# Kernel optimization log

Measured on AMD Instinct MI355X. Metric: run time of the kernel, lower is better.

The kernel has to match this reference:

```python
import jax, jax.numpy as jnp
import numpy as np

C = 256
R = 16  # reduction
CR = C // R
LN_EPS = 1e-5


def setup_inputs() -> dict:
    key = jax.random.key(0)
    ks = jax.random.split(key, 8)
    B, H, W = 16, 128, 128
    x = jax.random.normal(ks[0], (B, C, H, W), dtype=jnp.float32)
    # conv_mask: Conv2d(C, 1, 1x1)
    w_mask = jax.random.normal(ks[1], (C,), dtype=jnp.float32) * (1.0 / np.sqrt(C))
    b_mask = jnp.zeros((), dtype=jnp.float32)
    # channel_add[0]: Conv2d(C, C//R, 1x1)
    w1 = jax.random.normal(ks[2], (CR, C), dtype=jnp.float32) * (1.0 / np.sqrt(C))
    b1 = jnp.zeros((CR,), dtype=jnp.float32)
    # channel_add[1]: LayerNorm([C//R, 1, 1])
    ln_g = jnp.ones((CR,), dtype=jnp.float32)
    ln_b = jnp.zeros((CR,), dtype=jnp.float32)
    # channel_add[3]: Conv2d(C//R, C, 1x1)
    w2 = jax.random.normal(ks[3], (C, CR), dtype=jnp.float32) * (1.0 / np.sqrt(CR))
    b2 = jnp.zeros((C,), dtype=jnp.float32)
    return {"x": x, "w_mask": w_mask, "b_mask": b_mask,
            "w1": w1, "b1": b1, "ln_g": ln_g, "ln_b": ln_b,
            "w2": w2, "b2": b2}


def reference(x, w_mask, b_mask, w1, b1, ln_g, ln_b, w2, b2):
    B, Cc, H, W = x.shape
    # 1x1 conv to 1 channel -> attention logits over H*W
    logits = jnp.einsum('bchw,c->bhw', x, w_mask) + b_mask          # [B,H,W]
    attn = jax.nn.softmax(logits.reshape(B, H * W), axis=-1)        # [B,HW]
    # attention-pooled global context: [B,C]
    context = jnp.einsum('bchw,bs->bc', x, attn.reshape(B, H, W).reshape(B, H * W)[:, :].reshape(B, H * W)) if False else jnp.einsum('bcs,bs->bc', x.reshape(B, Cc, H * W), attn)
    # channel_add MLP: conv1x1 -> LayerNorm over [C//R] -> ReLU -> conv1x1
    t = jnp.einsum('oc,bc->bo', w1, context) + b1                   # [B,C//R]
    mu = jnp.mean(t, axis=-1, keepdims=True)
    var = jnp.mean((t - mu) ** 2, axis=-1, keepdims=True)
    t = (t - mu) / jnp.sqrt(var + LN_EPS) * ln_g + ln_b
    t = jax.nn.relu(t)
    add = jnp.einsum('oc,bc->bo', w2, t) + b2                       # [B,C]
    return x + add[:, :, None, None]
```

## Files before the change

### kernel.cpp

```cpp
#include <hip/hip_runtime.h>
#include <math.h>

#define CC   256
#define CR   16
#define SB   16384
#define NB   16
#define ST   64
#define NT   (SB/ST)
#define LN_EPS 1e-5f

typedef float vfloat4 __attribute__((ext_vector_type(4)));

__global__ __launch_bounds__(256) void k_ctx_partial(const float* __restrict__ x,
                                                     const float* __restrict__ w_mask,
                                                     float* __restrict__ pc,
                                                     float* __restrict__ pm,
                                                     float* __restrict__ ps) {
    __shared__ float plog[ST * 5];
    __shared__ float pl[ST];
    __shared__ float wm[CC];
    __shared__ float red2[CC * 17];

    const int t   = threadIdx.x;
    const int bid = blockIdx.x;
    const int b   = bid / NT;
    const int s0  = (bid % NT) * ST;

    wm[t] = w_mask[t];
    __syncthreads();

    const int g  = t >> 4;
    const int i  = t & 15;
    const int s4 = i << 2;

    const float* xb = x + (size_t)b * CC * SB + s0 + s4;
    float4 v[16];
    float4 acc = make_float4(0.f, 0.f, 0.f, 0.f);
#pragma unroll
    for (int k = 0; k < 16; ++k) {
        const int c = g + (k << 4);
        v[k] = *reinterpret_cast<const float4*>(xb + (size_t)c * SB);
        const float w = wm[c];
        acc.x += v[k].x * w; acc.y += v[k].y * w;
        acc.z += v[k].z * w; acc.w += v[k].w * w;
    }
    acc.x += __shfl_xor(acc.x, 16); acc.y += __shfl_xor(acc.y, 16);
    acc.z += __shfl_xor(acc.z, 16); acc.w += __shfl_xor(acc.w, 16);
    acc.x += __shfl_xor(acc.x, 32); acc.y += __shfl_xor(acc.y, 32);
    acc.z += __shfl_xor(acc.z, 32); acc.w += __shfl_xor(acc.w, 32);
    const int wv = t >> 6;
    if ((t & 63) < 16) {
        plog[(s4 + 0) * 5 + wv] = acc.x;
        plog[(s4 + 1) * 5 + wv] = acc.y;
        plog[(s4 + 2) * 5 + wv] = acc.z;
        plog[(s4 + 3) * 5 + wv] = acc.w;
    }
    __syncthreads();

    if (t < ST) {
        const float logit = plog[t * 5 + 0] + plog[t * 5 + 1]
                          + plog[t * 5 + 2] + plog[t * 5 + 3];
        float m = logit;
#pragma unroll
        for (int off = 32; off > 0; off >>= 1)
            m = fmaxf(m, __shfl_xor(m, off));
        const float p = __expf(logit - m);
        pl[t] = p;
        float sum = p;
#pragma unroll
        for (int off = 32; off > 0; off >>= 1)
            sum += __shfl_xor(sum, off);
        if (t == 0) { pm[bid] = m; ps[bid] = sum; }
    }
    __syncthreads();

    const float p0 = pl[s4 + 0], p1 = pl[s4 + 1];
    const float p2 = pl[s4 + 2], p3 = pl[s4 + 3];
#pragma unroll
    for (int k = 0; k < 16; ++k) {
        const int c = g + (k << 4);
        red2[c * 17 + i] = v[k].x * p0 + v[k].y * p1 + v[k].z * p2 + v[k].w * p3;
    }
    __syncthreads();

    float s = 0.f;
#pragma unroll
    for (int j = 0; j < 16; ++j) s += red2[t * 17 + j];
    pc[(size_t)bid * CC + t] = s;
}

__global__ __launch_bounds__(256) void k_combine_mlp(const float* __restrict__ pc,
                                                     const float* __restrict__ pm,
                                                     const float* __restrict__ ps,
                                                     const float* __restrict__ w1,
                                                     const float* __restrict__ b1,
                                                     const float* __restrict__ ln_g,
                                                     const float* __restrict__ ln_b,
                                                     const float* __restrict__ w2,
                                                     const float* __restrict__ b2,
                                                     float* __restrict__ add) {
    const int b = blockIdx.x;
    const int t = threadIdx.x;
    __shared__ float red[256];
    __shared__ float fx[NT];
    __shared__ float ctx[CC];
    __shared__ float tbuf[CR];
    __shared__ float tn[CR];

    const float m_t = pm[b * NT + t];
    red[t] = m_t; __syncthreads();
    for (int st = 128; st > 0; st >>= 1) {
        if (t < st) red[t] = fmaxf(red[t], red[t + st]);
        __syncthreads();
    }
    const float M = red[0]; __syncthreads();

    const float f = __expf(m_t - M);
    fx[t] = f;
    red[t] = ps[b * NT + t] * f; __syncthreads();
    for (int st = 128; st > 0; st >>= 1) {
        if (t < st) red[t] += red[t + st];
        __syncthreads();
    }
    const float invZ = 1.0f / red[0]; __syncthreads();

    float acc = 0.f;
#pragma unroll 4
    for (int j = 0; j < NT; ++j)
        acc += pc[((size_t)b * NT + j) * CC + t] * fx[j];
    ctx[t] = acc * invZ;
    __syncthreads();

    if (t < CR) {
        float a = b1[t];
        const float* w1r = w1 + (size_t)t * CC;
#pragma unroll 8
        for (int c = 0; c < CC; ++c) a += w1r[c] * ctx[c];
        tbuf[t] = a;
    }
    __syncthreads();
    if (t == 0) {
        float mu = 0.f;
        for (int i = 0; i < CR; ++i) mu += tbuf[i];
        mu *= (1.0f / CR);
        float var = 0.f;
        for (int i = 0; i < CR; ++i) { const float d = tbuf[i] - mu; var += d * d; }
        var *= (1.0f / CR);
        const float inv = rsqrtf(var + LN_EPS);
        for (int i = 0; i < CR; ++i) {
            const float v = (tbuf[i] - mu) * inv * ln_g[i] + ln_b[i];
            tn[i] = v > 0.f ? v : 0.f;
        }
    }
    __syncthreads();

    float a = b2[t];
    const float* w2r = w2 + (size_t)t * CR;
#pragma unroll
    for (int o = 0; o < CR; ++o) a += w2r[o] * tn[o];
    add[(size_t)b * CC + t] = a;
}

__global__ __launch_bounds__(256) void k_add(const float* __restrict__ x,
                                             const float* __restrict__ add,
                                             float* __restrict__ out) {
    const size_t idx = ((size_t)blockIdx.x * 256 + threadIdx.x) * 8;
    const size_t bc = idx / SB;
    const float a = add[bc];
    const float4 v0 = *reinterpret_cast<const float4*>(x + idx);
    const float4 v1 = *reinterpret_cast<const float4*>(x + idx + 4);
    vfloat4 o0 = {v0.x + a, v0.y + a, v0.z + a, v0.w + a};
    vfloat4 o1 = {v1.x + a, v1.y + a, v1.z + a, v1.w + a};
    __builtin_nontemporal_store(o0, reinterpret_cast<vfloat4*>(out + idx));
    __builtin_nontemporal_store(o1, reinterpret_cast<vfloat4*>(out + idx + 4));
}

extern "C" void kernel_launch(void* const* d_in, const int* in_sizes, int n_in,
                              void* d_out, int out_size, void* d_ws, size_t ws_size,
                              hipStream_t stream) {
    const float* x      = (const float*)d_in[0];
    const float* w_mask = (const float*)d_in[1];
    const float* w1     = (const float*)d_in[3];
    const float* b1     = (const float*)d_in[4];
    const float* ln_g   = (const float*)d_in[5];
    const float* ln_b   = (const float*)d_in[6];
    const float* w2     = (const float*)d_in[7];
    const float* b2     = (const float*)d_in[8];
    float* out = (float*)d_out;

    float* ws  = (float*)d_ws;
    float* pc  = ws;
    float* pm  = pc + (size_t)NB * NT * CC;
    float* ps  = pm + (size_t)NB * NT;
    float* add = ps + (size_t)NB * NT;

    k_ctx_partial<<<dim3(NB * NT), dim3(256), 0, stream>>>(x, w_mask, pc, pm, ps);
    k_combine_mlp<<<dim3(NB), dim3(256), 0, stream>>>(pc, pm, ps, w1, b1, ln_g, ln_b, w2, b2, add);
    k_add<<<dim3(NB * CC * SB / 2048), dim3(256), 0, stream>>>(x, add, out);
}
```

Measured before the change: 170.8 us.

## Restructure into six-kernel pipeline with bf16 copy of x for later passes

```diff
diff --git a/kernel.cpp b/kernel.cpp
--- a/kernel.cpp
+++ b/kernel.cpp
@@ -1,4 +1,5 @@
 #include <hip/hip_runtime.h>
+#include <hip/hip_bf16.h>
 #include <math.h>
 
 #define CC   256
@@ -7,11 +8,205 @@
 #define NB   16
 #define ST   64
 #define NT   (SB/ST)
+#define NCHUNK 64
+#define CHSZ  256
 #define LN_EPS 1e-5f
 
 typedef float vfloat4 __attribute__((ext_vector_type(4)));
 
-__global__ __launch_bounds__(256) void k_ctx_partial(const float* __restrict__ x,
+__device__ __forceinline__ unsigned short f2b(float f) {
+    __hip_bfloat16 h = __float2bfloat16(f);
+    unsigned short u;
+    __builtin_memcpy(&u, &h, 2);
+    return u;
+}
+__device__ __forceinline__ float b2f(unsigned short u) {
+    unsigned int v = ((unsigned int)u) << 16;
+    float f;
+    __builtin_memcpy(&f, &v, 4);
+    return f;
+}
+
+__global__ __launch_bounds__(256) void k1_logits_part(const float* __restrict__ x,
+                                                      const float* __restrict__ w_mask,
+                                                      __hip_bfloat16* __restrict__ xb16,
+                                                      float* __restrict__ part) {
+    const int t   = threadIdx.x;
+    const int bid = blockIdx.x;
+    const int sq  = bid & 3;
+    const int cg  = (bid >> 2) & 15;
+    const int b   = bid >> 6;
+
+    const size_t xoff = ((size_t)b * CC + (size_t)cg * 16) * SB + (size_t)sq * 4096;
+    const float* xb = x + xoff;
+    __hip_bfloat16* cb = xb16 + xoff;
+
+    float4 acc[4];
+#pragma unroll
+    for (int k = 0; k < 4; ++k) acc[k] = make_float4(0.f, 0.f, 0.f, 0.f);
+
+#pragma unroll 4
+    for (int c = 0; c < 16; ++c) {
+        const float w = w_mask[cg * 16 + c];
+#pragma unroll
+        for (int k = 0; k < 4; ++k) {
+            const float4 v = *reinterpret_cast<const float4*>(xb + (size_t)c * SB + k * 1024 + t * 4);
+            acc[k].x += w * v.x; acc[k].y += w * v.y;
+            acc[k].z += w * v.z; acc[k].w += w * v.w;
+            ushort4 u;
+            u.x = f2b(v.x); u.y = f2b(v.y); u.z = f2b(v.z); u.w = f2b(v.w);
+            *reinterpret_cast<ushort4*>(cb + (size_t)c * SB + k * 1024 + t * 4) = u;
+        }
+    }
+    float* pp = part + ((size_t)b * 16 + cg) * SB + (size_t)sq * 4096;
+#pragma unroll
+    for (int k = 0; k < 4; ++k)
+        *reinterpret_cast<float4*>(pp + k * 1024 + t * 4) = acc[k];
+}
+
+__global__ __launch_bounds__(256) void k2a_softmax_chunks(const float* __restrict__ part,
+                                                          float* __restrict__ pl_num,
+                                                          float* __restrict__ pm,
+                                                          float* __restrict__ ps) {
+    const int t  = threadIdx.x;
+    const int b  = blockIdx.x >> 6;
+    const int ch = blockIdx.x & 63;
+    __shared__ float red[256];
+
+    const int s = ch * CHSZ + t;
+    float l = 0.f;
+#pragma unroll 4
+    for (int cg = 0; cg < 16; ++cg)
+        l += part[((size_t)b * 16 + cg) * SB + s];
+
+    red[t] = l; __syncthreads();
+    for (int st = 128; st > 0; st >>= 1) {
+        if (t < st) red[t] = fmaxf(red[t], red[t + st]);
+        __syncthreads();
+    }
+    const float mc = red[0]; __syncthreads();
+
+    const float p = __expf(l - mc);
+    pl_num[(size_t)b * SB + s] = p;
+
+    red[t] = p; __syncthreads();
+    for (int st = 128; st > 0; st >>= 1) {
+        if (t < st) red[t] += red[t + st];
+        __syncthreads();
+    }
+    if (t == 0) { pm[b * NCHUNK + ch] = mc; ps[b * NCHUNK + ch] = red[0]; }
+}
+
+__global__ __launch_bounds__(64) void k2b_combine(const float* __restrict__ pm,
+                                                  const float* __restrict__ ps,
+                                                  float* __restrict__ fxn) {
+    const int b = blockIdx.x;
+    const int t = threadIdx.x;
+    const float m_t = pm[b * NCHUNK + t];
+    float M = m_t;
+#pragma unroll
+    for (int off = 32; off > 0; off >>= 1)
+        M = fmaxf(M, __shfl_xor(M, off));
+    const float f = __expf(m_t - M);
+    float z = ps[b * NCHUNK + t] * f;
+#pragma unroll
+    for (int off = 32; off > 0; off >>= 1)
+        z += __shfl_xor(z, off);
+    fxn[b * NCHUNK + t] = f / z;
+}
+
+__global__ __launch_bounds__(256) void k3_context(const __hip_bfloat16* __restrict__ xb16,
+                                                  const float* __restrict__ pl_num,
+                                                  const float* __restrict__ fxn,
+                                                  float* __restrict__ ctx) {
+    const int t = threadIdx.x;
+    const int b = blockIdx.x >> 8;
+    const int c = blockIdx.x & 255;
+    const __hip_bfloat16* row = xb16 + ((size_t)b * CC + c) * SB;
+    const float* pn = pl_num + (size_t)b * SB;
+    const float* fx = fxn + b * NCHUNK;
+
+    float acc = 0.f;
+#pragma unroll
+    for (int k = 0; k < 16; ++k) {
+        const int s = k * 1024 + t * 4;
+        const ushort4 u = *reinterpret_cast<const ushort4*>(row + s);
+        const float4 p = *reinterpret_cast<const float4*>(pn + s);
+        const float f = fx[s >> 8];
+        acc += f * (b2f(u.x) * p.x + b2f(u.y) * p.y + b2f(u.z) * p.z + b2f(u.w) * p.w);
+    }
+    __shared__ float red[256];
+    red[t] = acc; __syncthreads();
+    for (int st = 128; st > 0; st >>= 1) {
+        if (t < st) red[t] += red[t + st];
+        __syncthreads();
+    }
+    if (t == 0) ctx[(size_t)b * CC + c] = red[0];
+}
+
+__global__ __launch_bounds__(256) void k4_mlp(const float* __restrict__ ctx,
+                                              const float* __restrict__ w1,
+                                              const float* __restrict__ b1,
+                                              const float* __restrict__ ln_g,
+                                              const float* __restrict__ ln_b,
+                                              const float* __restrict__ w2,
+                                              const float* __restrict__ b2,
+                                              float* __restrict__ add) {
+    const int b = blockIdx.x;
+    const int t = threadIdx.x;
+    __shared__ float cx[CC];
+    __shared__ float tbuf[CR];
+    __shared__ float tn[CR];
+
+    cx[t] = ctx[(size_t)b * CC + t];
+    __syncthreads();
+
+    if (t < CR) {
+        float a = b1[t];
+        const float* w1r = w1 + (size_t)t * CC;
+#pragma unroll 8
+        for (int c = 0; c < CC; ++c) a += w1r[c] * cx[c];
+        tbuf[t] = a;
+    }
+    __syncthreads();
+    if (t == 0) {
+        float mu = 0.f;
+        for (int q = 0; q < CR; ++q) mu += tbuf[q];
+        mu *= (1.0f / CR);
+        float var = 0.f;
+        for (int q = 0; q < CR; ++q) { const float d = tbuf[q] - mu; var += d * d; }
+        var *= (1.0f / CR);
+        const float inv = rsqrtf(var + LN_EPS);
+        for (int q = 0; q < CR; ++q) {
+            const float v = (tbuf[q] - mu) * inv * ln_g[q] + ln_b[q];
+            tn[q] = v > 0.f ? v : 0.f;
+        }
+    }
+    __syncthreads();
+
+    float a = b2[t];
+    const float* w2r = w2 + (size_t)t * CR;
+#pragma unroll
+    for (int o = 0; o < CR; ++o) a += w2r[o] * tn[o];
+    add[(size_t)b * CC + t] = a;
+}
+
+__global__ __launch_bounds__(256) void k5_add(const __hip_bfloat16* __restrict__ xb16,
+                                              const float* __restrict__ add,
+                                              float* __restrict__ out) {
+    const size_t idx = ((size_t)blockIdx.x * 256 + threadIdx.x) * 8;
+    const size_t bc = idx / SB;
+    const float a = add[bc];
+    const uint4 d = *reinterpret_cast<const uint4*>(xb16 + idx);
+    vfloat4 o0 = {b2f(d.x & 0xffffu) + a, b2f(d.x >> 16) + a,
+                  b2f(d.y & 0xffffu) + a, b2f(d.y >> 16) + a};
+    vfloat4 o1 = {b2f(d.z & 0xffffu) + a, b2f(d.z >> 16) + a,
+                  b2f(d.w & 0xffffu) + a, b2f(d.w >> 16) + a};
+    __builtin_nontemporal_store(o0, reinterpret_cast<vfloat4*>(out + idx));
+    __builtin_nontemporal_store(o1, reinterpret_cast<vfloat4*>(out + idx + 4));
+}
+
+__global__ __launch_bounds__(256) void f_ctx_partial(const float* __restrict__ x,
                                                      const float* __restrict__ w_mask,
                                                      float* __restrict__ pc,
                                                      float* __restrict__ pm,
@@ -82,14 +277,13 @@
         red2[c * 17 + i] = v[k].x * p0 + v[k].y * p1 + v[k].z * p2 + v[k].w * p3;
     }
     __syncthreads();
-
     float s = 0.f;
 #pragma unroll
     for (int j = 0; j < 16; ++j) s += red2[t * 17 + j];
     pc[(size_t)bid * CC + t] = s;
 }
 
-__global__ __launch_bounds__(256) void k_combine_mlp(const float* __restrict__ pc,
+__global__ __launch_bounds__(256) void f_combine_mlp(const float* __restrict__ pc,
                                                      const float* __restrict__ pm,
                                                      const float* __restrict__ ps,
                                                      const float* __restrict__ w1,
@@ -161,7 +355,7 @@
     add[(size_t)b * CC + t] = a;
 }
 
-__global__ __launch_bounds__(256) void k_add(const float* __restrict__ x,
+__global__ __launch_bounds__(256) void f_add(const float* __restrict__ x,
                                              const float* __restrict__ add,
                                              float* __restrict__ out) {
     const size_t idx = ((size_t)blockIdx.x * 256 + threadIdx.x) * 8;
@@ -188,13 +382,32 @@
     const float* b2     = (const float*)d_in[8];
     float* out = (float*)d_out;
 
-    float* ws  = (float*)d_ws;
-    float* pc  = ws;
-    float* pm  = pc + (size_t)NB * NT * CC;
-    float* ps  = pm + (size_t)NB * NT;
-    float* add = ps + (size_t)NB * NT;
-
-    k_ctx_partial<<<dim3(NB * NT), dim3(256), 0, stream>>>(x, w_mask, pc, pm, ps);
-    k_combine_mlp<<<dim3(NB), dim3(256), 0, stream>>>(pc, pm, ps, w1, b1, ln_g, ln_b, w2, b2, add);
-    k_add<<<dim3(NB * CC * SB / 2048), dim3(256), 0, stream>>>(x, add, out);
-}
+    const size_t nx = (size_t)NB * CC * SB;
+    __hip_bfloat16* xb16 = (__hip_bfloat16*)d_ws;
+    float* fbase  = (float*)((char*)d_ws + nx * sizeof(__hip_bfloat16));
+    float* part   = fbase;
+    float* pl_num = part + (size_t)NB * 16 * SB;
+    float* pm     = pl_num + (size_t)NB * SB;
+    float* ps     = pm + NB * NCHUNK;
+    float* fxn    = ps + NB * NCHUNK;
+    float* ctx    = fxn + NB * NCHUNK;
+    float* add    = ctx + (size_t)NB * CC;
+    const size_t need = (size_t)((char*)(add + (size_t)NB * CC) - (char*)d_ws);
+
+    if (ws_size >= need) {
+        k1_logits_part<<<dim3(1024), dim3(256), 0, stream>>>(x, w_mask, xb16, part);
+        k2a_softmax_chunks<<<dim3(NB * NCHUNK), dim3(256), 0, stream>>>(part, pl_num, pm, ps);
+        k2b_combine<<<dim3(NB), dim3(64), 0, stream>>>(pm, ps, fxn);
+        k3_context<<<dim3(NB * CC), dim3(256), 0, stream>>>(xb16, pl_num, fxn, ctx);
+        k4_mlp<<<dim3(NB), dim3(256), 0, stream>>>(ctx, w1, b1, ln_g, ln_b, w2, b2, add);
+        k5_add<<<dim3(32768), dim3(256), 0, stream>>>(xb16, add, out);
+    } else {
+        float* pc  = (float*)d_ws;
+        float* fpm = pc + (size_t)NB * NT * CC;
+        float* fps = fpm + (size_t)NB * NT;
+        float* fad = fps + (size_t)NB * NT;
+        f_ctx_partial<<<dim3(NB * NT), dim3(256), 0, stream>>>(x, w_mask, pc, fpm, fps);
+        f_combine_mlp<<<dim3(NB), dim3(256), 0, stream>>>(pc, fpm, fps, w1, b1, ln_g, ln_b, w2, b2, fad);
+        f_add<<<dim3(NB * CC * SB / 2048), dim3(256), 0, stream>>>(x, fad, out);
+    }
+}
```

Measured after the change: 222.5 us. 30.2% more time.
